# Kernel tuning notes

Measured on AMD Instinct MI355X. Metric: run time of the kernel, lower is better.

The kernel has to match this reference:

```python
import functools
import jax, jax.numpy as jnp
import numpy as np

CUTOFF = 5.0
BOX = 80.0
N_POINTS = 8192
MAX_NEIGHBOURS = 32
MASK_VALUE = -1


def setup_inputs() -> dict:
    key = jax.random.key(0)
    positions = jax.random.uniform(key, (N_POINTS, 3), dtype=jnp.float32) * BOX
    return {"positions": positions, "max_neighbours": MAX_NEIGHBOURS}


def reference(positions, max_neighbours):
    # OpenBoundary.get_neighbours (include_self=False, cutoff=CUTOFF)
    n = positions.shape[0]
    # pairwise squared distances: vmap(neighbours_mask_direct) == full broadcast
    diff = positions[:, None, :] - positions[None, :, :]        # [N, N, 3]
    r2 = jnp.sum(diff * diff, axis=-1)                          # [N, N]
    neigh_mask = r2 <= CUTOFF * CUTOFF
    neigh_mask = neigh_mask & ~jnp.eye(n, dtype=bool)           # drop self
    # per-row compaction of hit indices into fixed-size buffer
    get_nb = functools.partial(jnp.argwhere, size=max_neighbours, fill_value=MASK_VALUE)
    to_idx = jax.vmap(get_nb)(neigh_mask)[..., 0]               # [N, max_neighbours]
    cell_indices = jnp.zeros((*to_idx.shape, 3), dtype=jnp.int32)
    actual_max_neighbours = jnp.max(neigh_mask.sum(axis=1))
    return to_idx, cell_indices, actual_max_neighbours
```

## Files before the change

### kernel.cpp

```cpp
#include <hip/hip_runtime.h>


constexpr int   N     = 8192;
constexpr int   MAXNB = 32;
constexpr float CUT2  = 25.0f;
constexpr int   C     = 16;
constexpr int   NCP   = C * C * C;
constexpr float INVW  = 0.2f;
constexpr int   QBLOCKS = N / 4;

__device__ __forceinline__ int cell_coord(float v) {
    int c = (int)(v * INVW);
    return c > C - 1 ? C - 1 : c;
}

__global__ __launch_bounds__(1024) void build_kernel(const float* __restrict__ pos,
                                                     int* __restrict__ start_g,
                                                     float4* __restrict__ sorted) {
    __shared__ int cnt[NCP];
    __shared__ int wsum[16];
    const int t    = threadIdx.x;
    const int lane = t & 63;
    const int wv   = t >> 6;

    #pragma unroll
    for (int k = t; k < NCP; k += 1024) cnt[k] = 0;
    __syncthreads();

    float x[8], y[8], z[8];
    int cid[8], rnk[8];
    #pragma unroll
    for (int q = 0; q < 8; ++q) {
        const int i = q * 1024 + t;
        x[q] = pos[3 * i + 0];
        y[q] = pos[3 * i + 1];
        z[q] = pos[3 * i + 2];
        cid[q] = (cell_coord(z[q]) << 8) | (cell_coord(y[q]) << 4) | cell_coord(x[q]);
        rnk[q] = atomicAdd(&cnt[cid[q]], 1);
    }
    __syncthreads();

    int c[4], pre[4], s0 = 0;
    #pragma unroll
    for (int k = 0; k < 4; ++k) { c[k] = cnt[4 * t + k]; pre[k] = s0; s0 += c[k]; }
    int inc = s0;
    #pragma unroll
    for (int off = 1; off < 64; off <<= 1) {
        const int v = __shfl_up(inc, off);
        if (lane >= off) inc += v;
    }
    if (lane == 63) wsum[wv] = inc;
    __syncthreads();
    if (t == 0) {
        int acc = 0;
        #pragma unroll
        for (int k = 0; k < 16; ++k) { const int tmp = wsum[k]; wsum[k] = acc; acc += tmp; }
    }
    __syncthreads();
    const int excl = wsum[wv] + (inc - s0);
    #pragma unroll
    for (int k = 0; k < 4; ++k) {
        cnt[4 * t + k]     = excl + pre[k];
        start_g[4 * t + k] = excl + pre[k];
    }
    if (t == 0) start_g[NCP] = N;
    __syncthreads();

    #pragma unroll
    for (int q = 0; q < 8; ++q) {
        const int p = cnt[cid[q]] + rnk[q];
        sorted[p] = make_float4(x[q], y[q], z[q], __int_as_float(q * 1024 + t));
    }
}

__global__ __launch_bounds__(256) void query_kernel(const float* __restrict__ pos,
                                                    const float4* __restrict__ sorted,
                                                    const int* __restrict__ start_g,
                                                    int* __restrict__ out_idx,
                                                    int4* __restrict__ cell4,
                                                    int* __restrict__ wavemax) {
    __shared__ int hitbuf[4][64];
    const int lane = threadIdx.x & 63;
    const int wave = threadIdx.x >> 6;

    if (threadIdx.x < 96) cell4[blockIdx.x * 96 + threadIdx.x] = make_int4(0, 0, 0, 0);

    const int p = __builtin_amdgcn_readfirstlane((int)blockIdx.x * 4 + wave);

    const float x = pos[3 * p + 0];
    const float y = pos[3 * p + 1];
    const float z = pos[3 * p + 2];
    const int cx = cell_coord(x), cy = cell_coord(y), cz = cell_coord(z);
    int xa = cx - 1; xa = xa < 0 ? 0 : (xa > C - 3 ? C - 3 : xa);
    int ya = cy - 1; ya = ya < 0 ? 0 : (ya > C - 3 ? C - 3 : ya);
    int za = cz - 1; za = za < 0 ? 0 : (za > C - 3 ? C - 3 : za);

    int bb[9], pre[10];
    pre[0] = 0;
    #pragma unroll
    for (int s = 0; s < 9; ++s) {
        const int rowb = ((za + s / 3) << 8) + ((ya + s % 3) << 4) + xa;
        bb[s] = start_g[rowb];
        pre[s + 1] = pre[s] + (start_g[rowb + 3] - bb[s]);
    }
    const int total = pre[9];

    int count = 0;
    int v = 0x7fffffff;

    if (total <= 64) {
        int idx = 0;
        #pragma unroll
        for (int s = 0; s < 9; ++s) {
            const bool in_s = (lane >= pre[s]) && (lane < pre[s + 1]);
            idx = in_s ? (bb[s] + (lane - pre[s])) : idx;
        }
        const float4 o = sorted[idx];
        const float dx = __fsub_rn(x, o.x);
        const float dy = __fsub_rn(y, o.y);
        const float dz = __fsub_rn(z, o.z);
        const float r2 = __fadd_rn(__fadd_rn(__fmul_rn(dx, dx), __fmul_rn(dy, dy)),
                                   __fmul_rn(dz, dz));
        const int j = __float_as_int(o.w);
        const bool hit = (lane < total) && (r2 <= CUT2) && (j != p);
        count = __popcll(__ballot(hit));
        v = hit ? j : 0x7fffffff;
    } else {
        for (int base = 0; base < total; base += 64) {
            const int l = base + lane;
            int idx = 0;
            #pragma unroll
            for (int s = 0; s < 9; ++s) {
                const bool in_s = (l >= pre[s]) && (l < pre[s + 1]);
                idx = in_s ? (bb[s] + (l - pre[s])) : idx;
            }
            const float4 o = sorted[idx];
            const float dx = __fsub_rn(x, o.x);
            const float dy = __fsub_rn(y, o.y);
            const float dz = __fsub_rn(z, o.z);
            const float r2 = __fadd_rn(__fadd_rn(__fmul_rn(dx, dx), __fmul_rn(dy, dy)),
                                       __fmul_rn(dz, dz));
            const int j = __float_as_int(o.w);
            const bool hit = (l < total) && (r2 <= CUT2) && (j != p);
            const unsigned long long m = __ballot(hit);
            if (hit) {
                const int pr = __builtin_amdgcn_mbcnt_hi(
                    (unsigned int)(m >> 32),
                    __builtin_amdgcn_mbcnt_lo((unsigned int)m, 0u));
                const int slot = count + pr;
                if (slot < 64) hitbuf[wave][slot] = j;
            }
            count += __popcll(m);
        }
        const int mcount = count < 64 ? count : 64;
        v = (lane < mcount) ? hitbuf[wave][lane] : 0x7fffffff;
    }

    #pragma unroll
    for (int k = 2; k <= 64; k <<= 1) {
        #pragma unroll
        for (int jj = k >> 1; jj >= 1; jj >>= 1) {
            const int pv = __shfl_xor(v, jj);
            const bool keepmin = ((lane & jj) == 0) == ((lane & k) == 0);
            v = keepmin ? min(v, pv) : max(v, pv);
        }
    }
    if (lane < MAXNB) out_idx[p * MAXNB + lane] = (lane < count) ? v : -1;

    if (lane == 0) wavemax[p] = count;
}

__global__ __launch_bounds__(1024) void maxred_kernel(const int* __restrict__ wavemax,
                                                      int* __restrict__ out_max) {
    __shared__ int wm[16];
    const int t    = threadIdx.x;
    const int lane = t & 63;
    const int wv   = t >> 6;
    const int4* w4 = (const int4*)wavemax;
    const int4 a = w4[t];
    const int4 b = w4[t + 1024];
    int mx = max(max(max(a.x, a.y), max(a.z, a.w)),
                 max(max(b.x, b.y), max(b.z, b.w)));
    #pragma unroll
    for (int off = 32; off > 0; off >>= 1) mx = max(mx, __shfl_xor(mx, off));
    if (lane == 0) wm[wv] = mx;
    __syncthreads();
    if (t == 0) {
        int m2 = wm[0];
        #pragma unroll
        for (int k = 1; k < 16; ++k) m2 = max(m2, wm[k]);
        *out_max = m2;
    }
}

extern "C" void kernel_launch(void* const* d_in, const int* in_sizes, int n_in,
                              void* d_out, int out_size, void* d_ws, size_t ws_size,
                              hipStream_t stream) {
    const float* pos = (const float*)d_in[0];
    int* out = (int*)d_out;

    int*  out_idx = out;
    int4* cell4   = (int4*)(out + N * MAXNB);
    int*  out_max = out + N * MAXNB * 4;

    char*   ws      = (char*)d_ws;
    float4* sorted  = (float4*)ws;
    int*    start_g = (int*)(ws + 131072);
    int*    wavemax = (int*)(ws + 147968);

    build_kernel <<<1, 1024, 0, stream>>>(pos, start_g, sorted);
    query_kernel <<<QBLOCKS, 256, 0, stream>>>(pos, sorted, start_g, out_idx, cell4, wavemax);
    maxred_kernel<<<1, 1024, 0, stream>>>(wavemax, out_max);
}
```

Measured before the change: 73.25 us.

## Replace cell-list neighbour search with brute-force all-pairs scan

Drops the single-block cell-binning build kernel and the cell-based query. In their place, a brute-force kernel has each wave handle four query points and scan all N candidates in index order, writing hits directly through ballot-based prefix slots. This removes the serial single-block build stage and the sort-based compaction, at the cost of O(N^2) distance work (8192×8192 pairs) instead of a local neighbourhood search. Because candidates are visited in ascending index order, the output is already sorted and no bitonic sort is needed.

```diff
diff --git a/kernel.cpp b/kernel.cpp
--- a/kernel.cpp
+++ b/kernel.cpp
@@ -4,170 +4,88 @@
 constexpr int   N     = 8192;
 constexpr int   MAXNB = 32;
 constexpr float CUT2  = 25.0f;
-constexpr int   C     = 16;
-constexpr int   NCP   = C * C * C;
-constexpr float INVW  = 0.2f;
-constexpr int   QBLOCKS = N / 4;
+constexpr int   BFBLOCKS = 512;
 
-__device__ __forceinline__ int cell_coord(float v) {
-    int c = (int)(v * INVW);
-    return c > C - 1 ? C - 1 : c;
+__device__ __forceinline__ int prefix_lt(unsigned long long m) {
+    return __builtin_amdgcn_mbcnt_hi((unsigned int)(m >> 32),
+                                     __builtin_amdgcn_mbcnt_lo((unsigned int)m, 0u));
 }
 
-__global__ __launch_bounds__(1024) void build_kernel(const float* __restrict__ pos,
-                                                     int* __restrict__ start_g,
-                                                     float4* __restrict__ sorted) {
-    __shared__ int cnt[NCP];
-    __shared__ int wsum[16];
-    const int t    = threadIdx.x;
-    const int lane = t & 63;
-    const int wv   = t >> 6;
-
-    #pragma unroll
-    for (int k = t; k < NCP; k += 1024) cnt[k] = 0;
-    __syncthreads();
-
-    float x[8], y[8], z[8];
-    int cid[8], rnk[8];
-    #pragma unroll
-    for (int q = 0; q < 8; ++q) {
-        const int i = q * 1024 + t;
-        x[q] = pos[3 * i + 0];
-        y[q] = pos[3 * i + 1];
-        z[q] = pos[3 * i + 2];
-        cid[q] = (cell_coord(z[q]) << 8) | (cell_coord(y[q]) << 4) | cell_coord(x[q]);
-        rnk[q] = atomicAdd(&cnt[cid[q]], 1);
-    }
-    __syncthreads();
-
-    int c[4], pre[4], s0 = 0;
-    #pragma unroll
-    for (int k = 0; k < 4; ++k) { c[k] = cnt[4 * t + k]; pre[k] = s0; s0 += c[k]; }
-    int inc = s0;
-    #pragma unroll
-    for (int off = 1; off < 64; off <<= 1) {
-        const int v = __shfl_up(inc, off);
-        if (lane >= off) inc += v;
-    }
-    if (lane == 63) wsum[wv] = inc;
-    __syncthreads();
-    if (t == 0) {
-        int acc = 0;
-        #pragma unroll
-        for (int k = 0; k < 16; ++k) { const int tmp = wsum[k]; wsum[k] = acc; acc += tmp; }
-    }
-    __syncthreads();
-    const int excl = wsum[wv] + (inc - s0);
-    #pragma unroll
-    for (int k = 0; k < 4; ++k) {
-        cnt[4 * t + k]     = excl + pre[k];
-        start_g[4 * t + k] = excl + pre[k];
-    }
-    if (t == 0) start_g[NCP] = N;
-    __syncthreads();
-
-    #pragma unroll
-    for (int q = 0; q < 8; ++q) {
-        const int p = cnt[cid[q]] + rnk[q];
-        sorted[p] = make_float4(x[q], y[q], z[q], __int_as_float(q * 1024 + t));
-    }
-}
-
-__global__ __launch_bounds__(256) void query_kernel(const float* __restrict__ pos,
-                                                    const float4* __restrict__ sorted,
-                                                    const int* __restrict__ start_g,
-                                                    int* __restrict__ out_idx,
-                                                    int4* __restrict__ cell4,
-                                                    int* __restrict__ wavemax) {
-    __shared__ int hitbuf[4][64];
+__global__ __launch_bounds__(256) void bf_kernel(const float* __restrict__ pos,
+                                                 int* __restrict__ out_idx,
+                                                 int4* __restrict__ cell4,
+                                                 int* __restrict__ wavemax) {
     const int lane = threadIdx.x & 63;
     const int wave = threadIdx.x >> 6;
 
-    if (threadIdx.x < 96) cell4[blockIdx.x * 96 + threadIdx.x] = make_int4(0, 0, 0, 0);
-
-    const int p = __builtin_amdgcn_readfirstlane((int)blockIdx.x * 4 + wave);
-
-    const float x = pos[3 * p + 0];
-    const float y = pos[3 * p + 1];
-    const float z = pos[3 * p + 2];
-    const int cx = cell_coord(x), cy = cell_coord(y), cz = cell_coord(z);
-    int xa = cx - 1; xa = xa < 0 ? 0 : (xa > C - 3 ? C - 3 : xa);
-    int ya = cy - 1; ya = ya < 0 ? 0 : (ya > C - 3 ? C - 3 : ya);
-    int za = cz - 1; za = za < 0 ? 0 : (za > C - 3 ? C - 3 : za);
-
-    int bb[9], pre[10];
-    pre[0] = 0;
-    #pragma unroll
-    for (int s = 0; s < 9; ++s) {
-        const int rowb = ((za + s / 3) << 8) + ((ya + s % 3) << 4) + xa;
-        bb[s] = start_g[rowb];
-        pre[s + 1] = pre[s] + (start_g[rowb + 3] - bb[s]);
-    }
-    const int total = pre[9];
-
-    int count = 0;
-    int v = 0x7fffffff;
-
-    if (total <= 64) {
-        int idx = 0;
-        #pragma unroll
-        for (int s = 0; s < 9; ++s) {
-            const bool in_s = (lane >= pre[s]) && (lane < pre[s + 1]);
-            idx = in_s ? (bb[s] + (lane - pre[s])) : idx;
-        }
-        const float4 o = sorted[idx];
-        const float dx = __fsub_rn(x, o.x);
-        const float dy = __fsub_rn(y, o.y);
-        const float dz = __fsub_rn(z, o.z);
-        const float r2 = __fadd_rn(__fadd_rn(__fmul_rn(dx, dx), __fmul_rn(dy, dy)),
-                                   __fmul_rn(dz, dz));
-        const int j = __float_as_int(o.w);
-        const bool hit = (lane < total) && (r2 <= CUT2) && (j != p);
-        count = __popcll(__ballot(hit));
-        v = hit ? j : 0x7fffffff;
-    } else {
-        for (int base = 0; base < total; base += 64) {
-            const int l = base + lane;
-            int idx = 0;
-            #pragma unroll
-            for (int s = 0; s < 9; ++s) {
-                const bool in_s = (l >= pre[s]) && (l < pre[s + 1]);
-                idx = in_s ? (bb[s] + (l - pre[s])) : idx;
-            }
-            const float4 o = sorted[idx];
-            const float dx = __fsub_rn(x, o.x);
-            const float dy = __fsub_rn(y, o.y);
-            const float dz = __fsub_rn(z, o.z);
-            const float r2 = __fadd_rn(__fadd_rn(__fmul_rn(dx, dx), __fmul_rn(dy, dy)),
-                                       __fmul_rn(dz, dz));
-            const int j = __float_as_int(o.w);
-            const bool hit = (l < total) && (r2 <= CUT2) && (j != p);
-            const unsigned long long m = __ballot(hit);
-            if (hit) {
-                const int pr = __builtin_amdgcn_mbcnt_hi(
-                    (unsigned int)(m >> 32),
-                    __builtin_amdgcn_mbcnt_lo((unsigned int)m, 0u));
-                const int slot = count + pr;
-                if (slot < 64) hitbuf[wave][slot] = j;
-            }
-            count += __popcll(m);
-        }
-        const int mcount = count < 64 ? count : 64;
-        v = (lane < mcount) ? hitbuf[wave][lane] : 0x7fffffff;
+    {
+        const int b = (int)blockIdx.x * 384;
+        cell4[b + threadIdx.x] = make_int4(0, 0, 0, 0);
+        if (threadIdx.x < 128) cell4[b + 256 + threadIdx.x] = make_int4(0, 0, 0, 0);
     }
 
-    #pragma unroll
-    for (int k = 2; k <= 64; k <<= 1) {
-        #pragma unroll
-        for (int jj = k >> 1; jj >= 1; jj >>= 1) {
-            const int pv = __shfl_xor(v, jj);
-            const bool keepmin = ((lane & jj) == 0) == ((lane & k) == 0);
-            v = keepmin ? min(v, pv) : max(v, pv);
+    const int w  = __builtin_amdgcn_readfirstlane((int)blockIdx.x * 4 + wave);
+    const int p0 = w * 4;
+    const float qx0 = pos[3 * p0 + 0], qy0 = pos[3 * p0 + 1], qz0 = pos[3 * p0 + 2];
+    const float qx1 = pos[3 * p0 + 3], qy1 = pos[3 * p0 + 4], qz1 = pos[3 * p0 + 5];
+    const float qx2 = pos[3 * p0 + 6], qy2 = pos[3 * p0 + 7], qz2 = pos[3 * p0 + 8];
+    const float qx3 = pos[3 * p0 + 9], qy3 = pos[3 * p0 + 10], qz3 = pos[3 * p0 + 11];
+
+    int c0 = 0, c1 = 0, c2 = 0, c3 = 0;
+
+    for (int base = 0; base < N; base += 64) {
+        const int j = base + lane;
+        const float cx = pos[3 * j + 0];
+        const float cy = pos[3 * j + 1];
+        const float cz = pos[3 * j + 2];
+
+        {
+            const float dx = __fsub_rn(qx0, cx), dy = __fsub_rn(qy0, cy), dz = __fsub_rn(qz0, cz);
+            const float r2 = __fadd_rn(__fadd_rn(__fmul_rn(dx, dx), __fmul_rn(dy, dy)), __fmul_rn(dz, dz));
+            const bool hit = (r2 <= CUT2) && (j != p0);
+            const unsigned long long m = __ballot(hit);
+            if (hit) { const int slot = c0 + prefix_lt(m); if (slot < MAXNB) out_idx[p0 * MAXNB + slot] = j; }
+            c0 += __popcll(m);
+        }
+        {
+            const float dx = __fsub_rn(qx1, cx), dy = __fsub_rn(qy1, cy), dz = __fsub_rn(qz1, cz);
+            const float r2 = __fadd_rn(__fadd_rn(__fmul_rn(dx, dx), __fmul_rn(dy, dy)), __fmul_rn(dz, dz));
+            const bool hit = (r2 <= CUT2) && (j != p0 + 1);
+            const unsigned long long m = __ballot(hit);
+            if (hit) { const int slot = c1 + prefix_lt(m); if (slot < MAXNB) out_idx[(p0 + 1) * MAXNB + slot] = j; }
+            c1 += __popcll(m);
+        }
+        {
+            const float dx = __fsub_rn(qx2, cx), dy = __fsub_rn(qy2, cy), dz = __fsub_rn(qz2, cz);
+            const float r2 = __fadd_rn(__fadd_rn(__fmul_rn(dx, dx), __fmul_rn(dy, dy)), __fmul_rn(dz, dz));
+            const bool hit = (r2 <= CUT2) && (j != p0 + 2);
+            const unsigned long long m = __ballot(hit);
+            if (hit) { const int slot = c2 + prefix_lt(m); if (slot < MAXNB) out_idx[(p0 + 2) * MAXNB + slot] = j; }
+            c2 += __popcll(m);
+        }
+        {
+            const float dx = __fsub_rn(qx3, cx), dy = __fsub_rn(qy3, cy), dz = __fsub_rn(qz3, cz);
+            const float r2 = __fadd_rn(__fadd_rn(__fmul_rn(dx, dx), __fmul_rn(dy, dy)), __fmul_rn(dz, dz));
+            const bool hit = (r2 <= CUT2) && (j != p0 + 3);
+            const unsigned long long m = __ballot(hit);
+            if (hit) { const int slot = c3 + prefix_lt(m); if (slot < MAXNB) out_idx[(p0 + 3) * MAXNB + slot] = j; }
+            c3 += __popcll(m);
         }
     }
-    if (lane < MAXNB) out_idx[p * MAXNB + lane] = (lane < count) ? v : -1;
 
-    if (lane == 0) wavemax[p] = count;
+    if (lane < MAXNB) {
+        if (lane >= c0) out_idx[p0 * MAXNB + lane] = -1;
+        if (lane >= c1) out_idx[(p0 + 1) * MAXNB + lane] = -1;
+        if (lane >= c2) out_idx[(p0 + 2) * MAXNB + lane] = -1;
+        if (lane >= c3) out_idx[(p0 + 3) * MAXNB + lane] = -1;
+    }
+
+    if (lane == 0) {
+        wavemax[p0]     = c0;
+        wavemax[p0 + 1] = c1;
+        wavemax[p0 + 2] = c2;
+        wavemax[p0 + 3] = c3;
+    }
 }
 
 __global__ __launch_bounds__(1024) void maxred_kernel(const int* __restrict__ wavemax,
@@ -203,12 +121,8 @@
     int4* cell4   = (int4*)(out + N * MAXNB);
     int*  out_max = out + N * MAXNB * 4;
 
-    char*   ws      = (char*)d_ws;
-    float4* sorted  = (float4*)ws;
-    int*    start_g = (int*)(ws + 131072);
-    int*    wavemax = (int*)(ws + 147968);
+    int* wavemax = (int*)d_ws;
 
-    build_kernel <<<1, 1024, 0, stream>>>(pos, start_g, sorted);
-    query_kernel <<<QBLOCKS, 256, 0, stream>>>(pos, sorted, start_g, out_idx, cell4, wavemax);
+    bf_kernel    <<<BFBLOCKS, 256, 0, stream>>>(pos, out_idx, cell4, wavemax);
     maxred_kernel<<<1, 1024, 0, stream>>>(wavemax, out_max);
 }
```

Result: slower. 117.1 us (+59.9%).

## Parallelize cell-list build across 64 blocks, one per cell range

Applied to the files above, without the earlier changes.

The single-block counting sort that builds the cell list is replaced by 64 blocks. Each block reads every position, counts points per 64-cell range and per cell within its own range, and scans both counts. It then writes the start offsets and sorted entries for its range only. This removes a serial bottleneck of one workgroup on a many-CU GPU, in exchange for every block redundantly reading all positions and counting range atomics.

```diff
diff --git a/kernel.cpp b/kernel.cpp
--- a/kernel.cpp
+++ b/kernel.cpp
@@ -8,27 +8,30 @@
 constexpr int   NCP   = C * C * C;
 constexpr float INVW  = 0.2f;
 constexpr int   QBLOCKS = N / 4;
+constexpr int   BBLK  = 64;
 
 __device__ __forceinline__ int cell_coord(float v) {
     int c = (int)(v * INVW);
     return c > C - 1 ? C - 1 : c;
 }
 
-__global__ __launch_bounds__(1024) void build_kernel(const float* __restrict__ pos,
-                                                     int* __restrict__ start_g,
-                                                     float4* __restrict__ sorted) {
-    __shared__ int cnt[NCP];
-    __shared__ int wsum[16];
+__global__ __launch_bounds__(1024) void buildp_kernel(const float* __restrict__ pos,
+                                                      int* __restrict__ start_g,
+                                                      float4* __restrict__ sorted) {
+    __shared__ int rangecnt[64];
+    __shared__ int cellcnt[64];
+    __shared__ int rangestart[64];
+    __shared__ int cellstart[64];
     const int t    = threadIdx.x;
     const int lane = t & 63;
     const int wv   = t >> 6;
-
-    #pragma unroll
-    for (int k = t; k < NCP; k += 1024) cnt[k] = 0;
+    const int r0   = (int)blockIdx.x;
+
+    if (t < 64) { rangecnt[t] = 0; cellcnt[t] = 0; }
     __syncthreads();
 
     float x[8], y[8], z[8];
-    int cid[8], rnk[8];
+    int cid[8], lrank[8];
     #pragma unroll
     for (int q = 0; q < 8; ++q) {
         const int i = q * 1024 + t;
@@ -36,40 +39,43 @@
         y[q] = pos[3 * i + 1];
         z[q] = pos[3 * i + 2];
         cid[q] = (cell_coord(z[q]) << 8) | (cell_coord(y[q]) << 4) | cell_coord(x[q]);
-        rnk[q] = atomicAdd(&cnt[cid[q]], 1);
-    }
-    __syncthreads();
-
-    int c[4], pre[4], s0 = 0;
-    #pragma unroll
-    for (int k = 0; k < 4; ++k) { c[k] = cnt[4 * t + k]; pre[k] = s0; s0 += c[k]; }
-    int inc = s0;
-    #pragma unroll
-    for (int off = 1; off < 64; off <<= 1) {
-        const int v = __shfl_up(inc, off);
-        if (lane >= off) inc += v;
-    }
-    if (lane == 63) wsum[wv] = inc;
-    __syncthreads();
-    if (t == 0) {
-        int acc = 0;
-        #pragma unroll
-        for (int k = 0; k < 16; ++k) { const int tmp = wsum[k]; wsum[k] = acc; acc += tmp; }
-    }
-    __syncthreads();
-    const int excl = wsum[wv] + (inc - s0);
-    #pragma unroll
-    for (int k = 0; k < 4; ++k) {
-        cnt[4 * t + k]     = excl + pre[k];
-        start_g[4 * t + k] = excl + pre[k];
-    }
-    if (t == 0) start_g[NCP] = N;
-    __syncthreads();
+        atomicAdd(&rangecnt[cid[q] >> 6], 1);
+        lrank[q] = ((cid[q] >> 6) == r0)
+                       ? atomicAdd(&cellcnt[cid[q] & 63], 1) : -1;
+    }
+    __syncthreads();
+
+    if (wv == 0) {
+        const int v = rangecnt[lane];
+        int inc = v;
+        #pragma unroll
+        for (int off = 1; off < 64; off <<= 1) {
+            const int u = __shfl_up(inc, off);
+            if (lane >= off) inc += u;
+        }
+        rangestart[lane] = inc - v;
+    } else if (wv == 1) {
+        const int v = cellcnt[lane];
+        int inc = v;
+        #pragma unroll
+        for (int off = 1; off < 64; off <<= 1) {
+            const int u = __shfl_up(inc, off);
+            if (lane >= off) inc += u;
+        }
+        cellstart[lane] = inc - v;
+    }
+    __syncthreads();
+
+    const int base = rangestart[r0];
+    if (t < 64) start_g[r0 * 64 + t] = base + cellstart[t];
+    if (r0 == BBLK - 1 && t == 0) start_g[NCP] = N;
 
     #pragma unroll
     for (int q = 0; q < 8; ++q) {
-        const int p = cnt[cid[q]] + rnk[q];
-        sorted[p] = make_float4(x[q], y[q], z[q], __int_as_float(q * 1024 + t));
+        if (lrank[q] >= 0) {
+            const int p = base + cellstart[cid[q] & 63] + lrank[q];
+            sorted[p] = make_float4(x[q], y[q], z[q], __int_as_float(q * 1024 + t));
+        }
     }
 }
 
@@ -208,7 +214,7 @@
     int*    start_g = (int*)(ws + 131072);
     int*    wavemax = (int*)(ws + 147968);
 
-    build_kernel <<<1, 1024, 0, stream>>>(pos, start_g, sorted);
+    buildp_kernel<<<BBLK, 1024, 0, stream>>>(pos, start_g, sorted);
     query_kernel <<<QBLOCKS, 256, 0, stream>>>(pos, sorted, start_g, out_idx, cell4, wavemax);
     maxred_kernel<<<1, 1024, 0, stream>>>(wavemax, out_max);
 }
```

Measured after the change: 68.46 us. 6.5% less time.
